# Optimization experiments

Measured on AMD Instinct MI355X. Metric: run time of the kernel, lower is better.

## Reference

```python
import jax, jax.numpy as jnp
import numpy as np

N = 50000      # nodes
E = 800000     # edges
F = 500        # num_features
HID = 64       # hidden_channels
H = 4          # num_heads
HC = HID // H  # headc = 16
C = 8          # num_classes
KHOP = 2       # K hops
CST = 1e-5


def setup_inputs() -> dict:
    key = jax.random.key(0)
    ks = jax.random.split(key, 12)
    s = 0.02
    return {
        "node_feat": jax.random.normal(ks[0], (N, F), dtype=jnp.float32),
        "edge_index": jax.random.randint(ks[1], (2, E), 0, N, dtype=jnp.int64),
        "Wi": jax.random.normal(ks[2], (F, HID), dtype=jnp.float32) * s,
        "bi": jnp.zeros((HID,), dtype=jnp.float32),
        "Wq": jax.random.normal(ks[3], (HID, H * HC), dtype=jnp.float32) * s,
        "bq": jnp.zeros((H * HC,), dtype=jnp.float32),
        "Wk": jax.random.normal(ks[4], (HID, H * HC), dtype=jnp.float32) * s,
        "bk": jnp.zeros((H * HC,), dtype=jnp.float32),
        "Wv": jax.random.normal(ks[5], (HID, H * C), dtype=jnp.float32) * s,
        "bv": jnp.zeros((H * C,), dtype=jnp.float32),
        "Wo": jax.random.normal(ks[6], (H * C, C), dtype=jnp.float32) * s,
        "bo": jnp.zeros((C,), dtype=jnp.float32),
        "hopwise": jnp.ones((KHOP + 1,), dtype=jnp.float32),
        "headwise": jnp.zeros((H, KHOP), dtype=jnp.float32),
        "teleport": jnp.ones((1,), dtype=jnp.float32),
    }


def reference(node_feat, edge_index, Wi, bi, Wq, bq, Wk, bk, Wv, bv, Wo, bo,
              hopwise, headwise, teleport):
    row, col = edge_index[0], edge_index[1]
    # degree(col): in-degree; norm = deg^-1 indexed at row (as in the torch code)
    deg = jax.ops.segment_sum(jnp.ones((E,), dtype=node_feat.dtype), col,
                              num_segments=N)
    deg_inv = jnp.where(deg > 0, 1.0 / deg, 0.0)  # [N]

    x = jax.nn.relu(node_feat @ Wi + bi)          # dropout p=0.0 / eval -> identity
    Q = (1.0 + jax.nn.elu(x @ Wq + bq)).reshape(N, H, HC)
    Kf = (1.0 + jax.nn.elu(x @ Wk + bk)).reshape(N, H, HC)
    V = (x @ Wv + bv).reshape(N, H, C)

    M = jnp.einsum('nhi,nhj->nhij', Kf, V)        # [N,H,HC,C]
    hidden = V * hopwise[0]                       # ind_gamma & gamma_softmax
    layerwise = jax.nn.softmax(headwise, axis=0)  # softmax over heads (dim=-2)

    # global attention (teleport) term
    teleportM = jnp.sum(M, axis=0, keepdims=True) / N      # [1,H,HC,C]
    teleportK = jnp.sum(Kf, axis=0, keepdims=True) / N     # [1,H,HC]
    teleportH = jnp.einsum('nhi,bhij->nhj', Q, teleportM)  # [N,H,C]
    teleportC = jnp.einsum('nhi,bhi->nh', Q, teleportK)[..., None] + CST
    teleportH = (teleportH / teleportC).sum(axis=-2)       # [N,C]

    for hop in range(KHOP):
        # norm[e] = deg_inv[row[e]]  =>  pre-scale source nodes, then scatter-add
        M = jax.ops.segment_sum((M * deg_inv[:, None, None, None])[row], col,
                                num_segments=N)
        Kf = jax.ops.segment_sum((Kf * deg_inv[:, None, None])[row], col,
                                 num_segments=N)
        Hh = jnp.einsum('nhi,nhij->nhj', Q, M)             # [N,H,C]
        Cc = jnp.einsum('nhi,nhi->nh', Q, Kf)[..., None] + CST
        gamma = hopwise[hop + 1] * layerwise[:, hop][:, None]  # [H,1]
        hidden = hidden + gamma * (Hh / Cc)

    # multi_concat output projection
    hidden = hidden.reshape(N, H * C) @ Wo + bo
    return hidden + teleport * teleportH
```

## Files before the change

### kernel.cpp

```cpp
#include <hip/hip_runtime.h>
#include <hip/hip_bf16.h>
#include <stdint.h>
#include <stddef.h>

#define NN 50000
#define NE 800000
#define FIN 500
#define HIDN 64
#define NH 4
#define HCD 16
#define NC 8
#define KVROW 192
#define SROW 640
#define CSTF 1e-5f
#define SCAN_NB 196
#define NTILES 782

typedef float f32x2 __attribute__((ext_vector_type(2)));
typedef __attribute__((ext_vector_type(8))) short bf16x8;
typedef __attribute__((ext_vector_type(4))) float f32x4;

__device__ inline float bf_lo(unsigned u) {
    union { unsigned i; float f; } v; v.i = u << 16; return v.f;
}
__device__ inline float bf_hi(unsigned u) {
    union { unsigned i; float f; } v; v.i = u & 0xffff0000u; return v.f;
}
__device__ inline unsigned short f2bf(float f) {
    union { float f; unsigned i; } v; v.f = f;
    unsigned r = v.i + 0x7fffu + ((v.i >> 16) & 1u);
    return (unsigned short)(r >> 16);
}
__device__ inline unsigned pack2bf(float a, float b) {
    __hip_bfloat162 h = __float22bfloat162_rn(make_float2(a, b));
    unsigned r; __builtin_memcpy(&r, &h, 4); return r;
}


__global__ void k_deg(const int* __restrict__ col, int* __restrict__ deg) {
    int e = blockIdx.x * blockDim.x + threadIdx.x;
    if (e < NE) atomicAdd(&deg[col[e]], 1);
}

__global__ void k_deginv(const int* __restrict__ deg, float* __restrict__ dinv,
                         int* __restrict__ cursor, float* __restrict__ tMK) {
    int i = blockIdx.x * blockDim.x + threadIdx.x;
    if (i < NN) {
        dinv[i] = deg[i] > 0 ? 1.0f / (float)deg[i] : 0.0f;
        cursor[i] = 0;
    }
    if (blockIdx.x == 0)
        for (int j = threadIdx.x; j < 576; j += 256) tMK[j] = 0.f;
}

__global__ void k_bsum(const int* __restrict__ deg, int* __restrict__ bsum) {
    __shared__ int red[256];
    int b = blockIdx.x, t = threadIdx.x;
    int i = b * 256 + t;
    red[t] = (i < NN) ? deg[i] : 0;
    __syncthreads();
    for (int d = 128; d > 0; d >>= 1) {
        if (t < d) red[t] += red[t + d];
        __syncthreads();
    }
    if (t == 0) bsum[b] = red[0];
}

__global__ void k_bscan(const int* __restrict__ bsum, int* __restrict__ bex) {
    __shared__ int s[256];
    int t = threadIdx.x;
    int own = (t < SCAN_NB) ? bsum[t] : 0;
    s[t] = own;
    __syncthreads();
    for (int d = 1; d < 256; d <<= 1) {
        int v = (t >= d) ? s[t - d] : 0;
        __syncthreads();
        s[t] += v;
        __syncthreads();
    }
    if (t < SCAN_NB) bex[t] = s[t] - own;
}

__global__ void k_expand(const int* __restrict__ deg, const int* __restrict__ bex,
                         int* __restrict__ offs) {
    __shared__ int s[256];
    int b = blockIdx.x, t = threadIdx.x;
    int i = b * 256 + t;
    int v = (i < NN) ? deg[i] : 0;
    s[t] = v;
    __syncthreads();
    for (int d = 1; d < 256; d <<= 1) {
        int a = (t >= d) ? s[t - d] : 0;
        __syncthreads();
        s[t] += a;
        __syncthreads();
    }
    int excl = s[t] - v + bex[b];
    if (i < NN) offs[i] = excl;
    if (i == NN - 1) offs[NN] = excl + v;
}

__global__ void k_scatter(const int* __restrict__ row, const int* __restrict__ col,
                          const int* __restrict__ offs, int* __restrict__ cursor,
                          int* __restrict__ csr_src) {
    int e = blockIdx.x * blockDim.x + threadIdx.x;
    if (e < NE) {
        int c = col[e];
        int pos = offs[c] + atomicAdd(&cursor[c], 1);
        csr_src[pos] = row[e];
    }
}


__global__ void k_wt(const float* __restrict__ Wi, unsigned short* __restrict__ Wt) {
    int i = blockIdx.x * blockDim.x + threadIdx.x;
    if (i < 64 * 512) {
        int c = i >> 9;
        int k = i & 511;
        Wt[i] = (k < FIN) ? f2bf(Wi[(size_t)k * 64 + c]) : (unsigned short)0;
    }
}


__global__ __launch_bounds__(256) void k_xgemm(const float* __restrict__ nf,
                                               const unsigned short* __restrict__ Wt,
                                               const float* __restrict__ bi,
                                               float* __restrict__ x) {
    int t = threadIdx.x;
    int lane = t & 63;
    int w = t >> 6;
    int quad = lane >> 4;
    int l15 = lane & 15;
    int n0 = blockIdx.x * 64;
    int rown = n0 + w * 16 + l15;
    const float* arow = &nf[(size_t)(rown < NN ? rown : 0) * FIN];

    f32x4 acc[4];
#pragma unroll
    for (int ct = 0; ct < 4; ct++) acc[ct] = (f32x4){0.f, 0.f, 0.f, 0.f};

    for (int k0 = 0; k0 < 512; k0 += 32) {
        int kk = k0 + quad * 8;
        float4 a0 = make_float4(0.f, 0.f, 0.f, 0.f);
        float4 a1 = make_float4(0.f, 0.f, 0.f, 0.f);
        if (kk < FIN) a0 = *(const float4*)&arow[kk];
        if (kk + 4 < FIN) a1 = *(const float4*)&arow[kk + 4];
        union { unsigned u[4]; bf16x8 v; } A;
        A.u[0] = pack2bf(a0.x, a0.y);
        A.u[1] = pack2bf(a0.z, a0.w);
        A.u[2] = pack2bf(a1.x, a1.y);
        A.u[3] = pack2bf(a1.z, a1.w);
#pragma unroll
        for (int ct = 0; ct < 4; ct++) {
            int c = ct * 16 + l15;
            bf16x8 bfr = *(const bf16x8*)&Wt[(size_t)c * 512 + kk];
            acc[ct] = __builtin_amdgcn_mfma_f32_16x16x32_bf16(A.v, bfr, acc[ct], 0, 0, 0);
        }
    }
#pragma unroll
    for (int ct = 0; ct < 4; ct++) {
        int c = ct * 16 + l15;
        float bv = bi[c];
#pragma unroll
        for (int r = 0; r < 4; r++) {
            int n = n0 + w * 16 + quad * 4 + r;
            if (n < NN)
                x[(size_t)n * 64 + c] = fmaxf(acc[ct][r] + bv, 0.f);
        }
    }
}


__global__ __launch_bounds__(256) void k_qkv(const float* __restrict__ x,
    const float* __restrict__ Wq, const float* __restrict__ bq,
    const float* __restrict__ Wk, const float* __restrict__ bk,
    const float* __restrict__ Wv, const float* __restrict__ bv,
    const float* __restrict__ hopwise, const float* __restrict__ dinv,
    float* __restrict__ Qg, float* __restrict__ hid,
    unsigned char* __restrict__ kv0, float* __restrict__ tMK) {
    __shared__ float wq_s[64 * 64], wk_s[64 * 64], wv_s[64 * 32];
    __shared__ float bq_s[64], bk_s[64], bv_s[32];
    __shared__ float xs[4][8][64];
    __shared__ float tacc[576];
    int t = threadIdx.x;
    for (int i = t; i < 4096; i += 256) { wq_s[i] = Wq[i]; wk_s[i] = Wk[i]; }
    for (int i = t; i < 2048; i += 256) wv_s[i] = Wv[i];
    if (t < 64) { bq_s[t] = bq[t]; bk_s[t] = bk[t]; }
    if (t >= 64 && t < 96) bv_s[t - 64] = bv[t - 64];
    for (int i = t; i < 576; i += 256) tacc[i] = 0.f;
    __syncthreads();
    int lane = t & 63;
    int w = t >> 6;
    int h = lane >> 4;
    int vcol = lane & 31;
    float hw0 = hopwise[0];
    float tkp = 0.f;
    float tmp_[8];
#pragma unroll
    for (int j = 0; j < 8; j++) tmp_[j] = 0.f;
    int tiles = (NN + 31) >> 5;
    for (int tile = blockIdx.x; tile < tiles; tile += gridDim.x) {
        int n0 = tile * 32 + w * 8;
        __syncthreads();
#pragma unroll
        for (int u = 0; u < 8; u++) {
            int n = n0 + u;
            xs[w][u][lane] = (n < NN) ? x[(size_t)n * 64 + lane] : 0.f;
        }
        __syncthreads();
        float aq[8], ak[8], av[8];
#pragma unroll
        for (int u = 0; u < 8; u++) { aq[u] = 0.f; ak[u] = 0.f; av[u] = 0.f; }
        for (int f = 0; f < 64; f++) {
            float wqv = wq_s[f * 64 + lane];
            float wkv = wk_s[f * 64 + lane];
            float wvv = wv_s[f * 32 + vcol];
#pragma unroll
            for (int u = 0; u < 8; u++) {
                float xf = xs[w][u][f];
                aq[u] = fmaf(xf, wqv, aq[u]);
                ak[u] = fmaf(xf, wkv, ak[u]);
                av[u] = fmaf(xf, wvv, av[u]);
            }
        }
#pragma unroll
        for (int u = 0; u < 8; u++) {
            int n = n0 + u;
            float q = aq[u] + bq_s[lane];
            float k = ak[u] + bk_s[lane];
            float v = av[u] + bv_s[vcol];
            float Qv = q > 0.f ? 1.f + q : expf(q);
            float Kv = k > 0.f ? 1.f + k : expf(k);
            if (n < NN) {
                Qg[(size_t)n * 64 + lane] = Qv;
                float vj[8];
#pragma unroll
                for (int j = 0; j < 8; j++) vj[j] = __shfl(v, h * 8 + j, 64);
                tkp += Kv;
#pragma unroll
                for (int j = 0; j < 8; j++) tmp_[j] += Kv * vj[j];
                float dv = dinv[n];
                unsigned short* kvrow = (unsigned short*)(kv0 + (size_t)n * KVROW);
                kvrow[lane] = f2bf(Kv * dv);
                if (lane < 32) kvrow[64 + lane] = f2bf(v);
                if (lane < 32) hid[(size_t)n * 32 + lane] = v * hw0;
            }
        }
    }
#pragma unroll
    for (int j = 0; j < 8; j++) atomicAdd(&tacc[lane * 8 + j], tmp_[j]);
    atomicAdd(&tacc[512 + lane], tkp);
    __syncthreads();
    for (int i = t; i < 576; i += 256) atomicAdd(&tMK[i], tacc[i]);
}


__global__ __launch_bounds__(256) void k_hop0(const unsigned char* __restrict__ kv0,
    const int* __restrict__ offs, const int* __restrict__ csr_src,
    const float* __restrict__ dinv, const float* __restrict__ Qg,
    const float* __restrict__ hopwise, const float* __restrict__ headwise,
    unsigned char* __restrict__ S1, float* __restrict__ hid) {
    int t = threadIdx.x;
    int lane = t & 63;
    int n = (blockIdx.x * 256 + t) >> 6;
    if (n >= NN) return;
    int h = lane >> 4;
    float e0 = expf(headwise[0]);
    float e1 = expf(headwise[2]);
    float e2 = expf(headwise[4]);
    float e3 = expf(headwise[6]);
    float esum = e0 + e1 + e2 + e3;
    float eh = (h == 0) ? e0 : ((h == 1) ? e1 : ((h == 2) ? e2 : e3));
    float gam = hopwise[1] * eh / esum;

    int hoff = 128 + h * 16;
    int o0 = offs[n], o1 = offs[n + 1];
    float kacc = 0.f;
    float4 m0 = make_float4(0.f, 0.f, 0.f, 0.f);
    float4 m1 = make_float4(0.f, 0.f, 0.f, 0.f);
    int e = o0;
    for (; e + 3 < o1; e += 4) {
        float kk_[4]; uint4 vv[4];
#pragma unroll
        for (int q = 0; q < 4; q++) {
            int s = csr_src[e + q];
            const unsigned char* r = kv0 + (size_t)s * KVROW;
            kk_[q] = bf_lo(((const unsigned short*)r)[lane]);
            vv[q] = *(const uint4*)(r + hoff);
        }
#pragma unroll
        for (int q = 0; q < 4; q++) {
            float ka = kk_[q]; uint4 va = vv[q];
            kacc += ka;
            m0.x = fmaf(ka, bf_lo(va.x), m0.x); m0.y = fmaf(ka, bf_hi(va.x), m0.y);
            m0.z = fmaf(ka, bf_lo(va.y), m0.z); m0.w = fmaf(ka, bf_hi(va.y), m0.w);
            m1.x = fmaf(ka, bf_lo(va.z), m1.x); m1.y = fmaf(ka, bf_hi(va.z), m1.y);
            m1.z = fmaf(ka, bf_lo(va.w), m1.z); m1.w = fmaf(ka, bf_hi(va.w), m1.w);
        }
    }
    for (; e < o1; e++) {
        int s = csr_src[e];
        const unsigned char* r = kv0 + (size_t)s * KVROW;
        float ka = bf_lo(((const unsigned short*)r)[lane]);
        uint4 va = *(const uint4*)(r + hoff);
        kacc += ka;
        m0.x = fmaf(ka, bf_lo(va.x), m0.x); m0.y = fmaf(ka, bf_hi(va.x), m0.y);
        m0.z = fmaf(ka, bf_lo(va.y), m0.z); m0.w = fmaf(ka, bf_hi(va.y), m0.w);
        m1.x = fmaf(ka, bf_lo(va.z), m1.x); m1.y = fmaf(ka, bf_hi(va.z), m1.y);
        m1.z = fmaf(ka, bf_lo(va.w), m1.z); m1.w = fmaf(ka, bf_hi(va.w), m1.w);
    }
    {
        float dv = dinv[n];
        float s16 = dv * 16.f;
        unsigned char* drow = S1 + (size_t)n * SROW;
        ((unsigned short*)drow)[lane] = f2bf(kacc * dv);
        unsigned u0 = __builtin_amdgcn_cvt_pk_fp8_f32(m0.x * s16, m0.y * s16, 0, false);
        u0 = __builtin_amdgcn_cvt_pk_fp8_f32(m0.z * s16, m0.w * s16, u0, true);
        unsigned u1 = __builtin_amdgcn_cvt_pk_fp8_f32(m1.x * s16, m1.y * s16, 0, false);
        u1 = __builtin_amdgcn_cvt_pk_fp8_f32(m1.z * s16, m1.w * s16, u1, true);
        uint2 pv; pv.x = u0; pv.y = u1;
        *(uint2*)(drow + 128 + lane * 8) = pv;
    }
    float qv = Qg[(size_t)n * 64 + lane];
    float hh[8];
    hh[0] = qv * m0.x; hh[1] = qv * m0.y; hh[2] = qv * m0.z; hh[3] = qv * m0.w;
    hh[4] = qv * m1.x; hh[5] = qv * m1.y; hh[6] = qv * m1.z; hh[7] = qv * m1.w;
    float cc = qv * kacc;
#pragma unroll
    for (int s = 1; s < 16; s <<= 1) {
#pragma unroll
        for (int j = 0; j < 8; j++) hh[j] += __shfl_xor(hh[j], s, 16);
        cc += __shfl_xor(cc, s, 16);
    }
    if ((lane & 15) < 8) {
        int j = lane & 7;
        float val = j < 4 ? (j < 2 ? (j == 0 ? hh[0] : hh[1]) : (j == 2 ? hh[2] : hh[3]))
                          : (j < 6 ? (j == 4 ? hh[4] : hh[5]) : (j == 6 ? hh[6] : hh[7]));
        size_t idx = (size_t)n * 32 + h * 8 + j;
        hid[idx] += gam * val / (cc + CSTF);
    }
}


__global__ __launch_bounds__(256) void k_prop1(const unsigned char* __restrict__ Sold,
    const int* __restrict__ offs, const int* __restrict__ csr_src,
    const float* __restrict__ Qg, const float* __restrict__ hopwise,
    const float* __restrict__ headwise, float* __restrict__ hid) {
    int t = threadIdx.x;
    int lane = t & 63;
    int n = (blockIdx.x * 256 + t) >> 6;
    if (n >= NN) return;
    int h = lane >> 4;
    float e0 = expf(headwise[1]);
    float e1 = expf(headwise[3]);
    float e2 = expf(headwise[5]);
    float e3 = expf(headwise[7]);
    float esum = e0 + e1 + e2 + e3;
    float eh = (h == 0) ? e0 : ((h == 1) ? e1 : ((h == 2) ? e2 : e3));
    float gam = hopwise[2] * eh / esum * 0.0625f;

    int o0 = offs[n], o1 = offs[n + 1];
    float kacc = 0.f;
    float4 m0 = make_float4(0.f, 0.f, 0.f, 0.f);
    float4 m1 = make_float4(0.f, 0.f, 0.f, 0.f);
    int e = o0;
    for (; e + 3 < o1; e += 4) {
        float kk_[4]; uint2 mv[4];
#pragma unroll
        for (int q = 0; q < 4; q++) {
            int s = csr_src[e + q];
            const unsigned char* r = Sold + (size_t)s * SROW;
            kk_[q] = bf_lo(((const unsigned short*)r)[lane]);
            mv[q] = *(const uint2*)(r + 128 + lane * 8);
        }
#pragma unroll
        for (int q = 0; q < 4; q++) {
            kacc += kk_[q];
            f32x2 a0 = __builtin_amdgcn_cvt_pk_f32_fp8(mv[q].x, false);
            f32x2 a1 = __builtin_amdgcn_cvt_pk_f32_fp8(mv[q].x, true);
            f32x2 b0 = __builtin_amdgcn_cvt_pk_f32_fp8(mv[q].y, false);
            f32x2 b1 = __builtin_amdgcn_cvt_pk_f32_fp8(mv[q].y, true);
            m0.x += a0.x; m0.y += a0.y; m0.z += a1.x; m0.w += a1.y;
            m1.x += b0.x; m1.y += b0.y; m1.z += b1.x; m1.w += b1.y;
        }
    }
    for (; e < o1; e++) {
        int s = csr_src[e];
        const unsigned char* r = Sold + (size_t)s * SROW;
        float ka = bf_lo(((const unsigned short*)r)[lane]);
        uint2 mva = *(const uint2*)(r + 128 + lane * 8);
        kacc += ka;
        f32x2 a0 = __builtin_amdgcn_cvt_pk_f32_fp8(mva.x, false);
        f32x2 a1 = __builtin_amdgcn_cvt_pk_f32_fp8(mva.x, true);
        f32x2 b0 = __builtin_amdgcn_cvt_pk_f32_fp8(mva.y, false);
        f32x2 b1 = __builtin_amdgcn_cvt_pk_f32_fp8(mva.y, true);
        m0.x += a0.x; m0.y += a0.y; m0.z += a1.x; m0.w += a1.y;
        m1.x += b0.x; m1.y += b0.y; m1.z += b1.x; m1.w += b1.y;
    }
    float qv = Qg[(size_t)n * 64 + lane];
    float hh[8];
    hh[0] = qv * m0.x; hh[1] = qv * m0.y; hh[2] = qv * m0.z; hh[3] = qv * m0.w;
    hh[4] = qv * m1.x; hh[5] = qv * m1.y; hh[6] = qv * m1.z; hh[7] = qv * m1.w;
    float cc = qv * kacc;
#pragma unroll
    for (int s = 1; s < 16; s <<= 1) {
#pragma unroll
        for (int j = 0; j < 8; j++) hh[j] += __shfl_xor(hh[j], s, 16);
        cc += __shfl_xor(cc, s, 16);
    }
    if ((lane & 15) < 8) {
        int j = lane & 7;
        float val = j < 4 ? (j < 2 ? (j == 0 ? hh[0] : hh[1]) : (j == 2 ? hh[2] : hh[3]))
                          : (j < 6 ? (j == 4 ? hh[4] : hh[5]) : (j == 6 ? hh[6] : hh[7]));
        size_t idx = (size_t)n * 32 + h * 8 + j;
        hid[idx] += gam * val / (cc + CSTF);
    }
}


__global__ __launch_bounds__(256) void k_final(const float* __restrict__ hid,
    const float* __restrict__ Qg, const float* __restrict__ Wo,
    const float* __restrict__ bo, const float* __restrict__ tMK,
    const float* __restrict__ teleport, float* __restrict__ out) {
    __shared__ float tm[512];
    __shared__ float tk[64];
    __shared__ float wo[256];
    __shared__ float bos[8];
    int t = threadIdx.x;
    const float invN = 1.0f / (float)NN;
    for (int i = t; i < 512; i += 256) tm[i] = tMK[i] * invN;
    if (t < 64) tk[t] = tMK[512 + t] * invN;
    wo[t] = Wo[t & 255];
    if (t < 8) bos[t] = bo[t];
    __syncthreads();
    float tp = teleport[0];
    int lane = t & 63;
    int sub = lane & 7;
    int g = lane >> 3;
    int wid = (blockIdx.x * 256 + t) >> 6;
    int nwaves = gridDim.x * 4;
    for (int nb = wid * 8; nb < NN; nb += nwaves * 8) {
        int n = nb + g;
        if (n < NN) {
            const float* hrow = hid + (size_t)n * 32;
            const float* qrow = Qg + (size_t)n * 64;
            float o = bos[sub];
#pragma unroll
            for (int m = 0; m < 32; m++) o = fmaf(hrow[m], wo[m * 8 + sub], o);
            float th = 0.f;
#pragma unroll
            for (int h2 = 0; h2 < 4; h2++) {
                float num = 0.f, den = 0.f;
#pragma unroll
                for (int i = 0; i < 16; i++) {
                    float q = qrow[h2 * 16 + i];
                    num = fmaf(q, tm[h2 * 128 + i * 8 + sub], num);
                    den = fmaf(q, tk[h2 * 16 + i], den);
                }
                th += num / (den + CSTF);
            }
            out[(size_t)n * 8 + sub] = o + tp * th;
        }
    }
}


extern "C" void kernel_launch(void* const* d_in, const int* in_sizes, int n_in,
                              void* d_out, int out_size, void* d_ws, size_t ws_size,
                              hipStream_t stream) {
    const float* nf = (const float*)d_in[0];
    const int* ei = (const int*)d_in[1];
    const float* Wi = (const float*)d_in[2];
    const float* bi = (const float*)d_in[3];
    const float* Wq = (const float*)d_in[4];
    const float* bq = (const float*)d_in[5];
    const float* Wk = (const float*)d_in[6];
    const float* bk = (const float*)d_in[7];
    const float* Wv = (const float*)d_in[8];
    const float* bv = (const float*)d_in[9];
    const float* Wo = (const float*)d_in[10];
    const float* bo = (const float*)d_in[11];
    const float* hopwise = (const float*)d_in[12];
    const float* headwise = (const float*)d_in[13];
    const float* teleport = (const float*)d_in[14];
    float* out = (float*)d_out;

    char* base = (char*)d_ws;
    size_t off = 0;
    auto alloc = [&](size_t bytes) -> void* {
        void* p = base + off;
        off = (off + bytes + 255) & ~(size_t)255;
        return p;
    };
    int* deg = (int*)alloc(NN * 4);
    int* cursor = (int*)alloc(NN * 4);
    int* offs = (int*)alloc((NN + 1) * 4);
    int* bsum = (int*)alloc(256 * 4);
    int* bex = (int*)alloc(256 * 4);
    float* dinv = (float*)alloc(NN * 4);
    int* csr_src = (int*)alloc((size_t)NE * 4);
    unsigned short* Wt = (unsigned short*)alloc(64 * 512 * 2);
    float* xbuf = (float*)alloc((size_t)NN * 64 * 4);
    float* Qg = (float*)alloc((size_t)NN * 64 * 4);
    float* hid = (float*)alloc((size_t)NN * 32 * 4);
    unsigned char* kv0 = (unsigned char*)alloc((size_t)NN * KVROW);
    unsigned char* S1 = (unsigned char*)alloc((size_t)NN * SROW);
    float* tMK = (float*)alloc(576 * 4);

    const int* rowp = ei;
    const int* colp = ei + NE;

    hipMemsetAsync(deg, 0, NN * 4, stream);

    k_deg<<<(NE + 255) / 256, 256, 0, stream>>>(colp, deg);
    k_deginv<<<(NN + 255) / 256, 256, 0, stream>>>(deg, dinv, cursor, tMK);
    k_bsum<<<SCAN_NB, 256, 0, stream>>>(deg, bsum);
    k_bscan<<<1, 256, 0, stream>>>(bsum, bex);
    k_expand<<<SCAN_NB, 256, 0, stream>>>(deg, bex, offs);
    k_scatter<<<(NE + 255) / 256, 256, 0, stream>>>(rowp, colp, offs, cursor, csr_src);
    k_wt<<<128, 256, 0, stream>>>(Wi, Wt);
    k_xgemm<<<NTILES, 256, 0, stream>>>(nf, Wt, bi, xbuf);
    k_qkv<<<512, 256, 0, stream>>>(xbuf, Wq, bq, Wk, bk, Wv, bv, hopwise, dinv,
                                   Qg, hid, kv0, tMK);
    k_hop0<<<(NN * 64 + 255) / 256, 256, 0, stream>>>(kv0, offs, csr_src, dinv, Qg,
                                                      hopwise, headwise, S1, hid);
    k_prop1<<<(NN * 64 + 255) / 256, 256, 0, stream>>>(S1, offs, csr_src, Qg,
                                                       hopwise, headwise, hid);
    k_final<<<1563, 256, 0, stream>>>(hid, Qg, Wo, bo, tMK, teleport, out);
}
```

Baseline: 480.6 us.

## Shrink hop state row to fp8 K, fuse setup kernels, widen gather unroll

The K accumulator in the hop-1 state row is stored as fp8 with a ×8 scale instead of bf16, shrinking SROW from 640 to 576 bytes and cutting gather traffic in k_prop1. The diff also merges k_deg with the Wi transpose and k_deginv into k_bsum to remove launches. It unrolls the gather loops to 8 edges, uses packed f32x2 math and readfirstlane on the node index, and raises the k_qkv grid to 768 blocks. The risks are lower precision on the propagated K sum and higher register pressure from the deeper unroll.

```diff
diff --git a/kernel.cpp b/kernel.cpp
--- a/kernel.cpp
+++ b/kernel.cpp
@@ -11,7 +11,7 @@
 #define HCD 16
 #define NC 8
 #define KVROW 192
-#define SROW 640
+#define SROW 576
 #define CSTF 1e-5f
 #define SCAN_NB 196
 #define NTILES 782
@@ -23,8 +23,10 @@
 __device__ inline float bf_lo(unsigned u) {
     union { unsigned i; float f; } v; v.i = u << 16; return v.f;
 }
-__device__ inline float bf_hi(unsigned u) {
-    union { unsigned i; float f; } v; v.i = u & 0xffff0000u; return v.f;
+__device__ inline f32x2 bfpair(unsigned u) {
+    union { unsigned i; float f; } lo, hi;
+    lo.i = u << 16; hi.i = u & 0xffff0000u;
+    f32x2 r; r.x = lo.f; r.y = hi.f; return r;
 }
 __device__ inline unsigned short f2bf(float f) {
     union { float f; unsigned i; } v; v.f = f;
@@ -37,30 +39,35 @@
 }
 
 
-__global__ void k_deg(const int* __restrict__ col, int* __restrict__ deg) {
+__global__ void k_deg_wt(const int* __restrict__ col, int* __restrict__ deg,
+                         const float* __restrict__ Wi, unsigned short* __restrict__ Wt) {
     int e = blockIdx.x * blockDim.x + threadIdx.x;
     if (e < NE) atomicAdd(&deg[col[e]], 1);
-}
-
-__global__ void k_deginv(const int* __restrict__ deg, float* __restrict__ dinv,
-                         int* __restrict__ cursor, float* __restrict__ tMK) {
-    int i = blockIdx.x * blockDim.x + threadIdx.x;
-    if (i < NN) {
-        dinv[i] = deg[i] > 0 ? 1.0f / (float)deg[i] : 0.0f;
-        cursor[i] = 0;
-    }
-    if (blockIdx.x == 0)
-        for (int j = threadIdx.x; j < 576; j += 256) tMK[j] = 0.f;
-}
-
-__global__ void k_bsum(const int* __restrict__ deg, int* __restrict__ bsum) {
+    if (e < 64 * 512) {
+        int c = e >> 9;
+        int k = e & 511;
+        Wt[e] = (k < FIN) ? f2bf(Wi[(size_t)k * 64 + c]) : (unsigned short)0;
+    }
+}
+
+
+__global__ void k_bsum(const int* __restrict__ deg, int* __restrict__ bsum,
+                       float* __restrict__ dinv, int* __restrict__ cursor,
+                       float* __restrict__ tMK) {
     __shared__ int red[256];
     int b = blockIdx.x, t = threadIdx.x;
     int i = b * 256 + t;
-    red[t] = (i < NN) ? deg[i] : 0;
+    int d = (i < NN) ? deg[i] : 0;
+    if (i < NN) {
+        dinv[i] = d > 0 ? 1.0f / (float)d : 0.0f;
+        cursor[i] = 0;
+    }
+    if (b == 0)
+        for (int j = t; j < 576; j += 256) tMK[j] = 0.f;
+    red[t] = d;
     __syncthreads();
-    for (int d = 128; d > 0; d >>= 1) {
-        if (t < d) red[t] += red[t + d];
+    for (int s = 128; s > 0; s >>= 1) {
+        if (t < s) red[t] += red[t + s];
         __syncthreads();
     }
     if (t == 0) bsum[b] = red[0];
@@ -108,16 +115,6 @@
         int c = col[e];
         int pos = offs[c] + atomicAdd(&cursor[c], 1);
         csr_src[pos] = row[e];
-    }
-}
-
-
-__global__ void k_wt(const float* __restrict__ Wi, unsigned short* __restrict__ Wt) {
-    int i = blockIdx.x * blockDim.x + threadIdx.x;
-    if (i < 64 * 512) {
-        int c = i >> 9;
-        int k = i & 511;
-        Wt[i] = (k < FIN) ? f2bf(Wi[(size_t)k * 64 + c]) : (unsigned short)0;
     }
 }
 
@@ -262,7 +259,7 @@
     unsigned char* __restrict__ S1, float* __restrict__ hid) {
     int t = threadIdx.x;
     int lane = t & 63;
-    int n = (blockIdx.x * 256 + t) >> 6;
+    int n = __builtin_amdgcn_readfirstlane((blockIdx.x * 256 + t) >> 6);
     if (n >= NN) return;
     int h = lane >> 4;
     float e0 = expf(headwise[0]);
@@ -276,26 +273,26 @@
     int hoff = 128 + h * 16;
     int o0 = offs[n], o1 = offs[n + 1];
     float kacc = 0.f;
-    float4 m0 = make_float4(0.f, 0.f, 0.f, 0.f);
-    float4 m1 = make_float4(0.f, 0.f, 0.f, 0.f);
+    f32x2 A0 = {0.f, 0.f}, A1 = {0.f, 0.f}, B0 = {0.f, 0.f}, B1 = {0.f, 0.f};
     int e = o0;
-    for (; e + 3 < o1; e += 4) {
-        float kk_[4]; uint4 vv[4];
-#pragma unroll
-        for (int q = 0; q < 4; q++) {
+    for (; e + 7 < o1; e += 8) {
+        float kk_[8]; uint4 vv[8];
+#pragma unroll
+        for (int q = 0; q < 8; q++) {
             int s = csr_src[e + q];
             const unsigned char* r = kv0 + (size_t)s * KVROW;
             kk_[q] = bf_lo(((const unsigned short*)r)[lane]);
             vv[q] = *(const uint4*)(r + hoff);
         }
 #pragma unroll
-        for (int q = 0; q < 4; q++) {
-            float ka = kk_[q]; uint4 va = vv[q];
+        for (int q = 0; q < 8; q++) {
+            float ka = kk_[q];
+            f32x2 ka2; ka2.x = ka; ka2.y = ka;
             kacc += ka;
-            m0.x = fmaf(ka, bf_lo(va.x), m0.x); m0.y = fmaf(ka, bf_hi(va.x), m0.y);
-            m0.z = fmaf(ka, bf_lo(va.y), m0.z); m0.w = fmaf(ka, bf_hi(va.y), m0.w);
-            m1.x = fmaf(ka, bf_lo(va.z), m1.x); m1.y = fmaf(ka, bf_hi(va.z), m1.y);
-            m1.z = fmaf(ka, bf_lo(va.w), m1.z); m1.w = fmaf(ka, bf_hi(va.w), m1.w);
+            A0 += ka2 * bfpair(vv[q].x);
+            A1 += ka2 * bfpair(vv[q].y);
+            B0 += ka2 * bfpair(vv[q].z);
+            B1 += ka2 * bfpair(vv[q].w);
         }
     }
     for (; e < o1; e++) {
@@ -303,28 +300,31 @@
         const unsigned char* r = kv0 + (size_t)s * KVROW;
         float ka = bf_lo(((const unsigned short*)r)[lane]);
         uint4 va = *(const uint4*)(r + hoff);
+        f32x2 ka2; ka2.x = ka; ka2.y = ka;
         kacc += ka;
-        m0.x = fmaf(ka, bf_lo(va.x), m0.x); m0.y = fmaf(ka, bf_hi(va.x), m0.y);
-        m0.z = fmaf(ka, bf_lo(va.y), m0.z); m0.w = fmaf(ka, bf_hi(va.y), m0.w);
-        m1.x = fmaf(ka, bf_lo(va.z), m1.x); m1.y = fmaf(ka, bf_hi(va.z), m1.y);
-        m1.z = fmaf(ka, bf_lo(va.w), m1.z); m1.w = fmaf(ka, bf_hi(va.w), m1.w);
+        A0 += ka2 * bfpair(va.x);
+        A1 += ka2 * bfpair(va.y);
+        B0 += ka2 * bfpair(va.z);
+        B1 += ka2 * bfpair(va.w);
     }
     {
         float dv = dinv[n];
+        float s8 = dv * 8.f;
         float s16 = dv * 16.f;
         unsigned char* drow = S1 + (size_t)n * SROW;
-        ((unsigned short*)drow)[lane] = f2bf(kacc * dv);
-        unsigned u0 = __builtin_amdgcn_cvt_pk_fp8_f32(m0.x * s16, m0.y * s16, 0, false);
-        u0 = __builtin_amdgcn_cvt_pk_fp8_f32(m0.z * s16, m0.w * s16, u0, true);
-        unsigned u1 = __builtin_amdgcn_cvt_pk_fp8_f32(m1.x * s16, m1.y * s16, 0, false);
-        u1 = __builtin_amdgcn_cvt_pk_fp8_f32(m1.z * s16, m1.w * s16, u1, true);
+        unsigned kb8 = __builtin_amdgcn_cvt_pk_fp8_f32(kacc * s8, 0.f, 0, false);
+        drow[lane] = (unsigned char)(kb8 & 0xff);
+        unsigned u0 = __builtin_amdgcn_cvt_pk_fp8_f32(A0.x * s16, A0.y * s16, 0, false);
+        u0 = __builtin_amdgcn_cvt_pk_fp8_f32(A1.x * s16, A1.y * s16, u0, true);
+        unsigned u1 = __builtin_amdgcn_cvt_pk_fp8_f32(B0.x * s16, B0.y * s16, 0, false);
+        u1 = __builtin_amdgcn_cvt_pk_fp8_f32(B1.x * s16, B1.y * s16, u1, true);
         uint2 pv; pv.x = u0; pv.y = u1;
-        *(uint2*)(drow + 128 + lane * 8) = pv;
+        *(uint2*)(drow + 64 + lane * 8) = pv;
     }
     float qv = Qg[(size_t)n * 64 + lane];
     float hh[8];
-    hh[0] = qv * m0.x; hh[1] = qv * m0.y; hh[2] = qv * m0.z; hh[3] = qv * m0.w;
-    hh[4] = qv * m1.x; hh[5] = qv * m1.y; hh[6] = qv * m1.z; hh[7] = qv * m1.w;
+    hh[0] = qv * A0.x; hh[1] = qv * A0.y; hh[2] = qv * A1.x; hh[3] = qv * A1.y;
+    hh[4] = qv * B0.x; hh[5] = qv * B0.y; hh[6] = qv * B1.x; hh[7] = qv * B1.y;
     float cc = qv * kacc;
 #pragma unroll
     for (int s = 1; s < 16; s <<= 1) {
@@ -348,7 +348,7 @@
     const float* __restrict__ headwise, float* __restrict__ hid) {
     int t = threadIdx.x;
     int lane = t & 63;
-    int n = (blockIdx.x * 256 + t) >> 6;
+    int n = __builtin_amdgcn_readfirstlane((blockIdx.x * 256 + t) >> 6);
     if (n >= NN) return;
     int h = lane >> 4;
     float e0 = expf(headwise[1]);
@@ -361,46 +361,44 @@
 
     int o0 = offs[n], o1 = offs[n + 1];
     float kacc = 0.f;
-    float4 m0 = make_float4(0.f, 0.f, 0.f, 0.f);
-    float4 m1 = make_float4(0.f, 0.f, 0.f, 0.f);
+    f32x2 A0 = {0.f, 0.f}, A1 = {0.f, 0.f}, B0 = {0.f, 0.f}, B1 = {0.f, 0.f};
     int e = o0;
-    for (; e + 3 < o1; e += 4) {
-        float kk_[4]; uint2 mv[4];
-#pragma unroll
-        for (int q = 0; q < 4; q++) {
+    for (; e + 7 < o1; e += 8) {
+        unsigned kb[8]; uint2 mv[8];
+#pragma unroll
+        for (int q = 0; q < 8; q++) {
             int s = csr_src[e + q];
             const unsigned char* r = Sold + (size_t)s * SROW;
-            kk_[q] = bf_lo(((const unsigned short*)r)[lane]);
-            mv[q] = *(const uint2*)(r + 128 + lane * 8);
-        }
-#pragma unroll
-        for (int q = 0; q < 4; q++) {
-            kacc += kk_[q];
-            f32x2 a0 = __builtin_amdgcn_cvt_pk_f32_fp8(mv[q].x, false);
-            f32x2 a1 = __builtin_amdgcn_cvt_pk_f32_fp8(mv[q].x, true);
-            f32x2 b0 = __builtin_amdgcn_cvt_pk_f32_fp8(mv[q].y, false);
-            f32x2 b1 = __builtin_amdgcn_cvt_pk_f32_fp8(mv[q].y, true);
-            m0.x += a0.x; m0.y += a0.y; m0.z += a1.x; m0.w += a1.y;
-            m1.x += b0.x; m1.y += b0.y; m1.z += b1.x; m1.w += b1.y;
+            kb[q] = r[lane];
+            mv[q] = *(const uint2*)(r + 64 + lane * 8);
+        }
+#pragma unroll
+        for (int q = 0; q < 8; q++) {
+            f32x2 kv = __builtin_amdgcn_cvt_pk_f32_fp8(kb[q], false);
+            kacc += kv.x;
+            A0 += __builtin_amdgcn_cvt_pk_f32_fp8(mv[q].x, false);
+            A1 += __builtin_amdgcn_cvt_pk_f32_fp8(mv[q].x, true);
+            B0 += __builtin_amdgcn_cvt_pk_f32_fp8(mv[q].y, false);
+            B1 += __builtin_amdgcn_cvt_pk_f32_fp8(mv[q].y, true);
         }
     }
     for (; e < o1; e++) {
         int s = csr_src[e];
         const unsigned char* r = Sold + (size_t)s * SROW;
-        float ka = bf_lo(((const unsigned short*)r)[lane]);
-        uint2 mva = *(const uint2*)(r + 128 + lane * 8);
-        kacc += ka;
-        f32x2 a0 = __builtin_amdgcn_cvt_pk_f32_fp8(mva.x, false);
-        f32x2 a1 = __builtin_amdgcn_cvt_pk_f32_fp8(mva.x, true);
-        f32x2 b0 = __builtin_amdgcn_cvt_pk_f32_fp8(mva.y, false);
-        f32x2 b1 = __builtin_amdgcn_cvt_pk_f32_fp8(mva.y, true);
-        m0.x += a0.x; m0.y += a0.y; m0.z += a1.x; m0.w += a1.y;
-        m1.x += b0.x; m1.y += b0.y; m1.z += b1.x; m1.w += b1.y;
-    }
+        unsigned kb = r[lane];
+        uint2 mva = *(const uint2*)(r + 64 + lane * 8);
+        f32x2 kv = __builtin_amdgcn_cvt_pk_f32_fp8(kb, false);
+        kacc += kv.x;
+        A0 += __builtin_amdgcn_cvt_pk_f32_fp8(mva.x, false);
+        A1 += __builtin_amdgcn_cvt_pk_f32_fp8(mva.x, true);
+        B0 += __builtin_amdgcn_cvt_pk_f32_fp8(mva.y, false);
+        B1 += __builtin_amdgcn_cvt_pk_f32_fp8(mva.y, true);
+    }
+    kacc *= 0.125f;
     float qv = Qg[(size_t)n * 64 + lane];
     float hh[8];
-    hh[0] = qv * m0.x; hh[1] = qv * m0.y; hh[2] = qv * m0.z; hh[3] = qv * m0.w;
-    hh[4] = qv * m1.x; hh[5] = qv * m1.y; hh[6] = qv * m1.z; hh[7] = qv * m1.w;
+    hh[0] = qv * A0.x; hh[1] = qv * A0.y; hh[2] = qv * A1.x; hh[3] = qv * A1.y;
+    hh[4] = qv * B0.x; hh[5] = qv * B0.y; hh[6] = qv * B1.x; hh[7] = qv * B1.y;
     float cc = qv * kacc;
 #pragma unroll
     for (int s = 1; s < 16; s <<= 1) {
@@ -512,15 +510,13 @@
 
     hipMemsetAsync(deg, 0, NN * 4, stream);
 
-    k_deg<<<(NE + 255) / 256, 256, 0, stream>>>(colp, deg);
-    k_deginv<<<(NN + 255) / 256, 256, 0, stream>>>(deg, dinv, cursor, tMK);
-    k_bsum<<<SCAN_NB, 256, 0, stream>>>(deg, bsum);
+    k_deg_wt<<<(NE + 255) / 256, 256, 0, stream>>>(colp, deg, Wi, Wt);
+    k_bsum<<<SCAN_NB, 256, 0, stream>>>(deg, bsum, dinv, cursor, tMK);
     k_bscan<<<1, 256, 0, stream>>>(bsum, bex);
     k_expand<<<SCAN_NB, 256, 0, stream>>>(deg, bex, offs);
     k_scatter<<<(NE + 255) / 256, 256, 0, stream>>>(rowp, colp, offs, cursor, csr_src);
-    k_wt<<<128, 256, 0, stream>>>(Wi, Wt);
     k_xgemm<<<NTILES, 256, 0, stream>>>(nf, Wt, bi, xbuf);
-    k_qkv<<<512, 256, 0, stream>>>(xbuf, Wq, bq, Wk, bk, Wv, bv, hopwise, dinv,
+    k_qkv<<<768, 256, 0, stream>>>(xbuf, Wq, bq, Wk, bk, Wv, bv, hopwise, dinv,
                                    Qg, hid, kv0, tMK);
     k_hop0<<<(NN * 64 + 255) / 256, 256, 0, stream>>>(kv0, offs, csr_src, dinv, Qg,
                                                       hopwise, headwise, S1, hid);
```

New measurement: 463.5 us. -3.6%, faster.
